# Optimization experiments

Measured on AMD Instinct MI355X. Metric: run time of the kernel, lower is better.

Reference implementation:

```python
import jax, jax.numpy as jnp
import numpy as np

# config
HIDDEN = 1024
NUM_EXPERTS = 16
TOP_K = 4
MOE_INTER = 512
NUM_SHARED = 2
SHARED_INTER = MOE_INTER * NUM_SHARED  # 1024
NORM_TOPK = True
ROUTED_SCALE = 1.0
NUM_TOKENS = 1024


def setup_inputs() -> dict:
    key = jax.random.key(0)
    ks = jax.random.split(key, 8)
    s = 0.02
    return {
        "hidden_states": jax.random.normal(ks[0], (NUM_TOKENS, HIDDEN), jnp.float32),
        # router (BailingMoEGate): weight [E, H], no bias
        "router_w": jax.random.normal(ks[1], (NUM_EXPERTS, HIDDEN), jnp.float32) * s,
        # routed experts: gate/up proj [E, H, I], down proj [E, I, H]
        "w_gate": jax.random.normal(ks[2], (NUM_EXPERTS, HIDDEN, MOE_INTER), jnp.float32) * s,
        "w_up": jax.random.normal(ks[3], (NUM_EXPERTS, HIDDEN, MOE_INTER), jnp.float32) * s,
        "w_down": jax.random.normal(ks[4], (NUM_EXPERTS, MOE_INTER, HIDDEN), jnp.float32) * s,
        # shared experts (BailingMoEMLP, merged gate_up): [H, 2*Is], [Is, H]
        "ws_gate_up": jax.random.normal(ks[5], (HIDDEN, 2 * SHARED_INTER), jnp.float32) * s,
        "ws_down": jax.random.normal(ks[6], (SHARED_INTER, HIDDEN), jnp.float32) * s,
    }


def _moe_forward(x, router_w, w_gate, w_up, w_down, ws_gate_up, ws_down):
    T = x.shape[0]
    # ---- router: logits -> softmax -> top-k (score_function='softmax', no bias)
    logits = jnp.einsum("th,eh->te", x, router_w)          # [T, E]
    probs = jax.nn.softmax(logits, axis=-1)
    topk_w, topk_idx = jax.lax.top_k(probs, TOP_K)         # [T, K]
    if NORM_TOPK:
        topk_w = topk_w / jnp.sum(topk_w, axis=-1, keepdims=True)
    topk_w = topk_w * ROUTED_SCALE
    # sparse combine weights [T, E] (zeros for non-selected experts)
    combine = jnp.zeros((T, NUM_EXPERTS), x.dtype).at[
        jnp.arange(T)[:, None], topk_idx
    ].set(topk_w.astype(x.dtype))
    # ---- routed experts: SiLU(x W_gate) * (x W_up) then W_down, weighted combine
    g = jnp.einsum("th,ehi->tei", x, w_gate)               # [T, E, I]
    u = jnp.einsum("th,ehi->tei", x, w_up)
    h = jax.nn.silu(g) * u
    routed = jnp.einsum("tei,eih,te->th", h, w_down, combine)
    # ---- shared experts (dense SwiGLU MLP)
    gu = x @ ws_gate_up                                    # [T, 2*Is]
    g_s, u_s = jnp.split(gu, 2, axis=-1)
    shared = (jax.nn.silu(g_s) * u_s) @ ws_down
    return routed + shared


def reference(hidden_states, router_w, w_gate, w_up, w_down, ws_gate_up, ws_down):
    return _moe_forward(hidden_states, router_w, w_gate, w_up, w_down,
                        ws_gate_up, ws_down)
```

## Files before the change

kernel.cpp:

```cpp
#include <hip/hip_runtime.h>
#include <stdint.h>


typedef __attribute__((ext_vector_type(8))) unsigned short ushort8;
typedef __attribute__((ext_vector_type(4))) float f32x4;
typedef __attribute__((ext_vector_type(8))) __bf16 bf16x8;

#define T_TOK 1024
#define HID   1024
#define NEXP  16
#define TOPK  4
#define MINTER 512
#define SINTER 1024

constexpr size_t WGU_E = 32 * 1024 * 32;
constexpr size_t WD_E  = 16 * 1024 * 32;

constexpr size_t OFF_COUNTS = 0;
constexpr size_t OFF_LIST   = 1024;
constexpr size_t OFF_WT     = OFF_LIST  + 65536;
constexpr size_t OFF_TIDX   = OFF_WT    + 65536;
constexpr size_t OFF_XB     = OFF_TIDX  + 65536;
constexpr size_t OFF_HR     = OFF_XB    + 2097152;
constexpr size_t OFF_HS     = OFF_HR    + 4194304;
constexpr size_t OFF_WGU    = OFF_HS    + 2097152;
constexpr size_t OFF_WD     = OFF_WGU   + 33554432;
constexpr size_t OFF_WSGU   = OFF_WD    + 16777216;
constexpr size_t OFF_WSD    = OFF_WSGU  + 4194304;
constexpr size_t OFF_ROUT   = OFF_WGU;

__device__ __forceinline__ unsigned short f2bf(float f) {
  union { float f; uint32_t u; } v; v.f = f;
  uint32_t r = (v.u + 0x7FFFu + ((v.u >> 16) & 1u)) >> 16;
  return (unsigned short)r;
}
__device__ __forceinline__ float bfu2f(uint32_t u) {
  union { uint32_t u; float f; } v; v.u = u << 16; return v.f;
}
__device__ __forceinline__ bf16x8 as_bf16x8(ushort8 s) {
  union { ushort8 s; bf16x8 b; } u; u.s = s; return u.b;
}
__device__ __forceinline__ float silu(float g) { return g / (1.f + __expf(-g)); }

__device__ __forceinline__ void glds16(const unsigned short* g, unsigned short* l) {
  __builtin_amdgcn_global_load_lds(
      (const __attribute__((address_space(1))) unsigned int*)g,
      (__attribute__((address_space(3))) unsigned int*)l, 16, 0, 0);
}

#define PIPE_BARRIER3() asm volatile("s_waitcnt vmcnt(3) lgkmcnt(0)\ns_barrier" ::: "memory")
#define PIPE_BARRIER0() asm volatile("s_waitcnt vmcnt(0) lgkmcnt(0)\ns_barrier" ::: "memory")

__global__ void init_kernel(int* counts) {
  if (threadIdx.x < NEXP) counts[threadIdx.x] = 0;
}

__global__ __launch_bounds__(64) void router_kernel(
    const float* __restrict__ x, const float* __restrict__ rw,
    int* counts, int* list, float* wt, int* tIdx,
    unsigned short* __restrict__ Xb) {
  const int t = blockIdx.x, l = threadIdx.x;
  float xv[16];
#pragma unroll
  for (int j = 0; j < 16; j++) xv[j] = x[t * HID + j * 64 + l];
#pragma unroll
  for (int j = 0; j < 16; j++) Xb[t * HID + j * 64 + l] = f2bf(xv[j]);
  float p[NEXP];
#pragma unroll
  for (int e = 0; e < NEXP; e++) {
    float s = 0.f;
#pragma unroll
    for (int j = 0; j < 16; j++) s += xv[j] * rw[e * HID + j * 64 + l];
#pragma unroll
    for (int off = 32; off > 0; off >>= 1) s += __shfl_xor(s, off);
    p[e] = s;
  }
  float mx = p[0];
#pragma unroll
  for (int e = 1; e < NEXP; e++) mx = fmaxf(mx, p[e]);
  int idx[TOPK]; float w4[TOPK]; float wsum = 0.f; unsigned used = 0u;
#pragma unroll
  for (int k = 0; k < TOPK; k++) {
    float bv = -1e30f; int bi = 0;
#pragma unroll
    for (int e = 0; e < NEXP; e++)
      if (!((used >> e) & 1u) && p[e] > bv) { bv = p[e]; bi = e; }
    used |= 1u << bi;
    idx[k] = bi;
    w4[k] = __expf(p[bi] - mx);
    wsum += w4[k];
  }
  const float inv = 1.f / wsum;
  if (l < TOPK) {
    const int e = idx[l];
    const int pos = atomicAdd(&counts[e], 1);
    list[e * 1024 + pos] = t;
    wt[e * 1024 + pos]   = w4[l] * inv;
    tIdx[t * TOPK + l]   = (e << 10) | pos;
  }
}

__global__ __launch_bounds__(256) void pack_all_kernel(
    const float* __restrict__ Wg, const float* __restrict__ Wu,
    const float* __restrict__ Wd, const float* __restrict__ Wsgu,
    const float* __restrict__ Wsd,
    unsigned short* __restrict__ WGUp, unsigned short* __restrict__ WDp,
    unsigned short* __restrict__ WSGUp, unsigned short* __restrict__ WSDp) {
  const int bid = blockIdx.x;
  const float* src; unsigned short* dst; int C, Nj, kp0, r0, c0, jbase, ilv;
  if (bid < 2048) {
    const int e = bid >> 7, loc = bid & 127, kt = loc >> 3, nt = loc & 7;
    src = Wg + (size_t)e * HID * MINTER; dst = WGUp + (size_t)e * WGU_E;
    C = MINTER; Nj = 1024; kp0 = 2 * kt; r0 = 64 * kt; c0 = 64 * nt;
    jbase = 128 * nt; ilv = 1;
  } else if (bid < 4096) {
    const int e = (bid - 2048) >> 7, loc = bid & 127, kt = loc >> 3, nt = loc & 7;
    src = Wu + (size_t)e * HID * MINTER; dst = WGUp + (size_t)e * WGU_E;
    C = MINTER; Nj = 1024; kp0 = 2 * kt; r0 = 64 * kt; c0 = 64 * nt;
    jbase = 128 * nt + 16; ilv = 1;
  } else if (bid < 6144) {
    const int e = (bid - 4096) >> 7, loc = bid & 127, kt = loc >> 4, nt = loc & 15;
    src = Wd + (size_t)e * MINTER * HID; dst = WDp + (size_t)e * WD_E;
    C = HID; Nj = 1024; kp0 = 2 * kt; r0 = 64 * kt; c0 = 64 * nt;
    jbase = 64 * nt; ilv = 0;
  } else if (bid < 6656) {
    const int loc = bid - 6144, kt = loc >> 5, nt = loc & 31;
    src = Wsgu; dst = WSGUp;
    C = 2048; Nj = 2048; kp0 = 2 * kt; r0 = 64 * kt; c0 = 64 * nt;
    const int isU = (nt >= 16), ntc = nt & 15;
    jbase = 128 * ntc + 16 * isU; ilv = 1;
  } else {
    const int loc = bid - 6656, kt = loc >> 4, nt = loc & 15;
    src = Wsd; dst = WSDp;
    C = HID; Nj = 1024; kp0 = 2 * kt; r0 = 64 * kt; c0 = 64 * nt;
    jbase = 64 * nt; ilv = 0;
  }
  __shared__ float tile[64][65];
  const int t = threadIdx.x;
  {
    const int r = t >> 4, c4 = (t & 15) * 4;
#pragma unroll
    for (int p = 0; p < 4; p++) {
      const int rr = p * 16 + r;
      const float4 v = *(const float4*)(src + (size_t)(r0 + rr) * C + c0 + c4);
      tile[rr][c4 + 0] = v.x; tile[rr][c4 + 1] = v.y;
      tile[rr][c4 + 2] = v.z; tile[rr][c4 + 3] = v.w;
    }
  }
  __syncthreads();
  {
    const int n = t >> 2, k8 = (t & 3) * 8;
    const int j = jbase + (ilv ? (32 * (n >> 4) + (n & 15)) : n);
#pragma unroll
    for (int h = 0; h < 2; h++) {
      const int k = 32 * h + k8;
      union { unsigned short u[8]; ushort8 v; } pk;
#pragma unroll
      for (int i = 0; i < 8; i++) pk.u[i] = f2bf(tile[k + i][n]);
      *(ushort8*)(dst + ((size_t)(kp0 + h) * Nj + j) * 32 + k8) = pk.v;
    }
  }
}

__global__ __launch_bounds__(256, 4) void phase1_kernel(
    const unsigned short* __restrict__ Xb,
    const unsigned short* __restrict__ WGUp,
    const unsigned short* __restrict__ WSGUp,
    const int* __restrict__ counts, const int* __restrict__ list,
    const float* __restrict__ wt,
    unsigned short* __restrict__ Hr,
    unsigned short* __restrict__ Hs) {
  const int z = blockIdx.z, x = blockIdx.x, y = blockIdx.y;
  const bool routed = (z < NEXP);
  int cnt = 0, base = 0;
  if (routed) {
    if (x >= 16) return;
    cnt = counts[z];
    if (y * 128 >= cnt) return;
#pragma unroll
    for (int i = 0; i < NEXP; i++) base += (i < z) ? counts[i] : 0;
  }
  __shared__ __align__(16) unsigned short sA[3][128 * 32];
  __shared__ __align__(16) unsigned short sB[3][64 * 32];
  const int tid = threadIdx.x, w = tid >> 6, l = tid & 63;
  const int wm = w >> 1, wn = w & 1, m0 = y * 128;
  const int swz = ((l & 3) ^ ((l >> 3) & 3)) * 8;
  const int Nj = routed ? 1024 : 2048;

  const unsigned short* aS[2];
#pragma unroll
  for (int ii = 0; ii < 2; ii++) {
    const int r = 32 * w + 16 * ii + (l >> 2);
    const unsigned short* row = routed
        ? Xb + (size_t)list[z * 1024 + min(m0 + r, cnt - 1)] * HID
        : Xb + (size_t)(m0 + r) * HID;
    aS[ii] = row + swz;
  }
  const unsigned short* pan = routed ? WGUp + (size_t)z * WGU_E : WSGUp;
  const unsigned short* bS = pan + ((size_t)(x * 64 + 16 * w + (l >> 2))) * 32 + swz;
  const size_t bStep = (size_t)Nj * 32;

  const int rsw = ((l >> 4) ^ (((l & 15) >> 1) & 3)) * 8;
  int aOff[4], bOff[2];
#pragma unroll
  for (int i = 0; i < 4; i++) aOff[i] = (wm * 64 + 16 * i + (l & 15)) * 32 + rsw;
#pragma unroll
  for (int jt = 0; jt < 2; jt++) bOff[jt] = (wn * 32 + 16 * jt + (l & 15)) * 32 + rsw;

  f32x4 acc[4][2];
#pragma unroll
  for (int i = 0; i < 4; i++)
#pragma unroll
    for (int jt = 0; jt < 2; jt++) acc[i][jt] = (f32x4){0.f, 0.f, 0.f, 0.f};

  auto stage = [&](int s, int b) {
    glds16(aS[0] + s * 32, &sA[b][(32 * w) * 32]);
    glds16(aS[1] + s * 32, &sA[b][(32 * w + 16) * 32]);
    glds16(bS + s * bStep, &sB[b][(16 * w) * 32]);
  };

  const int steps = HID / 32;
  stage(0, 0); stage(1, 1);
#pragma unroll 1
  for (int s = 0; s < steps; s++) {
    const int cb = s % 3;
    if (s + 2 < steps) { PIPE_BARRIER3(); stage(s + 2, (s + 2) % 3); }
    else if (s + 1 < steps) { PIPE_BARRIER3(); }
    else { PIPE_BARRIER0(); }
    const unsigned short* A = &sA[cb][0];
    const unsigned short* B = &sB[cb][0];
    bf16x8 af[4], bfr[2];
#pragma unroll
    for (int i = 0; i < 4; i++) af[i] = as_bf16x8(*(const ushort8*)(A + aOff[i]));
#pragma unroll
    for (int jt = 0; jt < 2; jt++) bfr[jt] = as_bf16x8(*(const ushort8*)(B + bOff[jt]));
#pragma unroll
    for (int jt = 0; jt < 2; jt++)
#pragma unroll
      for (int i = 0; i < 4; i++)
        acc[i][jt] = __builtin_amdgcn_mfma_f32_16x16x32_bf16(af[i], bfr[jt], acc[i][jt], 0, 0, 0);
  }

  const int rl = (l >> 4) * 4, pc = 16 * wn + (l & 15);
#pragma unroll
  for (int i = 0; i < 4; i++)
#pragma unroll
    for (int r = 0; r < 4; r++) {
      const int grow = m0 + wm * 64 + 16 * i + rl + r;
      const float g = acc[i][0][r], u = acc[i][1][r];
      if (routed) {
        if (grow < cnt) {
          const float h = silu(g) * u * wt[z * 1024 + grow];
          Hr[((size_t)x * 4096 + base + grow) * 32 + pc] = f2bf(h);
        }
      } else {
        const float h = silu(g) * u;
        Hs[((size_t)x * 1024 + grow) * 32 + pc] = f2bf(h);
      }
    }
}

__global__ __launch_bounds__(256, 4) void phase2_kernel(
    const unsigned short* __restrict__ Hr, const unsigned short* __restrict__ Hs,
    const unsigned short* __restrict__ WDp, const unsigned short* __restrict__ WSDp,
    const int* __restrict__ counts,
    unsigned short* __restrict__ Rout,
    float* __restrict__ out) {
  const int z = blockIdx.z, x = blockIdx.x, y = blockIdx.y;
  const bool routed = (z < NEXP);
  int cnt = 0, base = 0, steps;
  if (routed) {
    cnt = counts[z];
    if (y * 128 >= cnt) return;
#pragma unroll
    for (int i = 0; i < NEXP; i++) base += (i < z) ? counts[i] : 0;
    steps = MINTER / 32;
  } else {
    steps = SINTER / 32;
  }
  __shared__ __align__(16) unsigned short sA[3][128 * 32];
  __shared__ __align__(16) unsigned short sB[3][64 * 32];
  const int tid = threadIdx.x, w = tid >> 6, l = tid & 63;
  const int wm = w >> 1, wn = w & 1, m0 = y * 128;
  const int swz = ((l & 3) ^ ((l >> 3) & 3)) * 8;
  const size_t aStep = (size_t)(routed ? 4096 : 1024) * 32;

  const unsigned short* aS[2];
#pragma unroll
  for (int ii = 0; ii < 2; ii++) {
    const int r = 32 * w + 16 * ii + (l >> 2);
    const int R = routed ? (base + min(m0 + r, cnt - 1)) : (m0 + r);
    aS[ii] = (routed ? Hr : Hs) + (size_t)R * 32 + swz;
  }
  const unsigned short* pan = routed ? WDp + (size_t)z * WD_E : WSDp;
  const unsigned short* bS = pan + ((size_t)(x * 64 + 16 * w + (l >> 2))) * 32 + swz;
  const size_t bStep = (size_t)1024 * 32;

  const int rsw = ((l >> 4) ^ (((l & 15) >> 1) & 3)) * 8;
  int aOff[4], bOff[2];
#pragma unroll
  for (int i = 0; i < 4; i++) aOff[i] = (wm * 64 + 16 * i + (l & 15)) * 32 + rsw;
#pragma unroll
  for (int jt = 0; jt < 2; jt++) bOff[jt] = (wn * 32 + 16 * jt + (l & 15)) * 32 + rsw;

  f32x4 acc[4][2];
#pragma unroll
  for (int i = 0; i < 4; i++)
#pragma unroll
    for (int jt = 0; jt < 2; jt++) acc[i][jt] = (f32x4){0.f, 0.f, 0.f, 0.f};

  auto stage = [&](int s, int b) {
    glds16(aS[0] + s * aStep, &sA[b][(32 * w) * 32]);
    glds16(aS[1] + s * aStep, &sA[b][(32 * w + 16) * 32]);
    glds16(bS + s * bStep, &sB[b][(16 * w) * 32]);
  };

  stage(0, 0); stage(1, 1);
#pragma unroll 1
  for (int s = 0; s < steps; s++) {
    const int cb = s % 3;
    if (s + 2 < steps) { PIPE_BARRIER3(); stage(s + 2, (s + 2) % 3); }
    else if (s + 1 < steps) { PIPE_BARRIER3(); }
    else { PIPE_BARRIER0(); }
    const unsigned short* A = &sA[cb][0];
    const unsigned short* B = &sB[cb][0];
    bf16x8 af[4], bfr[2];
#pragma unroll
    for (int i = 0; i < 4; i++) af[i] = as_bf16x8(*(const ushort8*)(A + aOff[i]));
#pragma unroll
    for (int jt = 0; jt < 2; jt++) bfr[jt] = as_bf16x8(*(const ushort8*)(B + bOff[jt]));
#pragma unroll
    for (int jt = 0; jt < 2; jt++)
#pragma unroll
      for (int i = 0; i < 4; i++)
        acc[i][jt] = __builtin_amdgcn_mfma_f32_16x16x32_bf16(af[i], bfr[jt], acc[i][jt], 0, 0, 0);
  }

  const int rl = (l >> 4) * 4;
#pragma unroll
  for (int i = 0; i < 4; i++)
#pragma unroll
    for (int r = 0; r < 4; r++) {
      const int grow = m0 + wm * 64 + 16 * i + rl + r;
#pragma unroll
      for (int jt = 0; jt < 2; jt++) {
        const int col = 64 * x + 32 * wn + 16 * jt + (l & 15);
        if (routed) {
          if (grow < cnt)
            Rout[(size_t)(base + grow) * HID + col] = f2bf(acc[i][jt][r]);
        } else {
          out[(size_t)grow * HID + col] = acc[i][jt][r];
        }
      }
    }
}

__global__ __launch_bounds__(256) void combine_kernel(
    const unsigned short* __restrict__ Rout, const int* __restrict__ counts,
    const int* __restrict__ tIdx, float* __restrict__ out) {
  __shared__ int sb[NEXP];
  if (threadIdx.x == 0) {
    int s = 0;
#pragma unroll
    for (int e = 0; e < NEXP; e++) { sb[e] = s; s += counts[e]; }
  }
  __syncthreads();
  const int t = blockIdx.x, c4 = threadIdx.x * 4;
  float4 o = *(const float4*)(out + (size_t)t * HID + c4);
#pragma unroll
  for (int k = 0; k < TOPK; k++) {
    const int v = tIdx[t * TOPK + k];
    const int row = sb[v >> 10] + (v & 1023);
    const uint2 rv = *(const uint2*)(Rout + (size_t)row * HID + c4);
    o.x += bfu2f(rv.x & 0xffffu); o.y += bfu2f(rv.x >> 16);
    o.z += bfu2f(rv.y & 0xffffu); o.w += bfu2f(rv.y >> 16);
  }
  *(float4*)(out + (size_t)t * HID + c4) = o;
}

extern "C" void kernel_launch(void* const* d_in, const int* in_sizes, int n_in,
                              void* d_out, int out_size, void* d_ws, size_t ws_size,
                              hipStream_t stream) {
  const float* x      = (const float*)d_in[0];
  const float* rw     = (const float*)d_in[1];
  const float* w_gate = (const float*)d_in[2];
  const float* w_up   = (const float*)d_in[3];
  const float* w_down = (const float*)d_in[4];
  const float* ws_gu  = (const float*)d_in[5];
  const float* ws_dn  = (const float*)d_in[6];
  float* out = (float*)d_out;
  char* ws = (char*)d_ws;

  int*   counts = (int*)  (ws + OFF_COUNTS);
  int*   list   = (int*)  (ws + OFF_LIST);
  float* wtbuf  = (float*)(ws + OFF_WT);
  int*   tIdx   = (int*)  (ws + OFF_TIDX);
  unsigned short* Xb    = (unsigned short*)(ws + OFF_XB);
  unsigned short* Hr    = (unsigned short*)(ws + OFF_HR);
  unsigned short* Hs    = (unsigned short*)(ws + OFF_HS);
  unsigned short* WGUp  = (unsigned short*)(ws + OFF_WGU);
  unsigned short* WDp   = (unsigned short*)(ws + OFF_WD);
  unsigned short* WSGUp = (unsigned short*)(ws + OFF_WSGU);
  unsigned short* WSDp  = (unsigned short*)(ws + OFF_WSD);
  unsigned short* Rout  = (unsigned short*)(ws + OFF_ROUT);

  init_kernel<<<1, 64, 0, stream>>>(counts);
  router_kernel<<<T_TOK, 64, 0, stream>>>(x, rw, counts, list, wtbuf, tIdx, Xb);
  pack_all_kernel<<<6912, 256, 0, stream>>>(
      w_gate, w_up, w_down, ws_gu, ws_dn, WGUp, WDp, WSGUp, WSDp);
  phase1_kernel<<<dim3(32, 8, 17), 256, 0, stream>>>(
      Xb, WGUp, WSGUp, counts, list, wtbuf, Hr, Hs);
  phase2_kernel<<<dim3(16, 8, 17), 256, 0, stream>>>(
      Hr, Hs, WDp, WSDp, counts, Rout, out);
  combine_kernel<<<T_TOK, 256, 0, stream>>>(Rout, counts, tIdx, out);
  (void)in_sizes; (void)n_in; (void)out_size; (void)ws_size;
}
```

Before: 243.4 us.

## Shrink GEMM tiles to 64x64 with 2-wave blocks and 4-stage pipeline

Both expert GEMM kernels drop from 128x64 tiles with 4 waves to 64x64 tiles with 2 waves per block, doubling the y grid. The global-to-LDS pipeline deepens from 3 to 4 buffers with matching vmcnt waits. The aim is finer granularity for experts with few tokens, less padding waste and more blocks to fill the CUs. In exchange, each block reuses the weight tiles across fewer rows, so weight traffic from memory and L2 rises.

Measured after the change: 261.4 us. 1.07x slower.

```diff
diff --git a/kernel.cpp b/kernel.cpp
--- a/kernel.cpp
+++ b/kernel.cpp
@@ -48,7 +48,8 @@
       (__attribute__((address_space(3))) unsigned int*)l, 16, 0, 0);
 }
 
-#define PIPE_BARRIER3() asm volatile("s_waitcnt vmcnt(3) lgkmcnt(0)\ns_barrier" ::: "memory")
+#define PIPE_BARRIER8() asm volatile("s_waitcnt vmcnt(8) lgkmcnt(0)\ns_barrier" ::: "memory")
+#define PIPE_BARRIER4() asm volatile("s_waitcnt vmcnt(4) lgkmcnt(0)\ns_barrier" ::: "memory")
 #define PIPE_BARRIER0() asm volatile("s_waitcnt vmcnt(0) lgkmcnt(0)\ns_barrier" ::: "memory")
 
 __global__ void init_kernel(int* counts) {
@@ -162,7 +163,7 @@
   }
 }
 
-__global__ __launch_bounds__(256, 4) void phase1_kernel(
+__global__ __launch_bounds__(128, 3) void phase1_kernel(
     const unsigned short* __restrict__ Xb,
     const unsigned short* __restrict__ WGUp,
     const unsigned short* __restrict__ WSGUp,
@@ -176,14 +177,14 @@
   if (routed) {
     if (x >= 16) return;
     cnt = counts[z];
-    if (y * 128 >= cnt) return;
+    if (y * 64 >= cnt) return;
 #pragma unroll
     for (int i = 0; i < NEXP; i++) base += (i < z) ? counts[i] : 0;
   }
-  __shared__ __align__(16) unsigned short sA[3][128 * 32];
-  __shared__ __align__(16) unsigned short sB[3][64 * 32];
+  __shared__ __align__(16) unsigned short sA[4][64 * 32];
+  __shared__ __align__(16) unsigned short sB[4][64 * 32];
   const int tid = threadIdx.x, w = tid >> 6, l = tid & 63;
-  const int wm = w >> 1, wn = w & 1, m0 = y * 128;
+  const int wn = w, m0 = y * 64;
   const int swz = ((l & 3) ^ ((l >> 3) & 3)) * 8;
   const int Nj = routed ? 1024 : 2048;
 
@@ -197,15 +198,18 @@
     aS[ii] = row + swz;
   }
   const unsigned short* pan = routed ? WGUp + (size_t)z * WGU_E : WSGUp;
-  const unsigned short* bS = pan + ((size_t)(x * 64 + 16 * w + (l >> 2))) * 32 + swz;
+  const unsigned short* bS[2];
+#pragma unroll
+  for (int ii = 0; ii < 2; ii++)
+    bS[ii] = pan + ((size_t)(x * 64 + 32 * w + 16 * ii + (l >> 2))) * 32 + swz;
   const size_t bStep = (size_t)Nj * 32;
 
   const int rsw = ((l >> 4) ^ (((l & 15) >> 1) & 3)) * 8;
   int aOff[4], bOff[2];
 #pragma unroll
-  for (int i = 0; i < 4; i++) aOff[i] = (wm * 64 + 16 * i + (l & 15)) * 32 + rsw;
-#pragma unroll
-  for (int jt = 0; jt < 2; jt++) bOff[jt] = (wn * 32 + 16 * jt + (l & 15)) * 32 + rsw;
+  for (int i = 0; i < 4; i++) aOff[i] = (16 * i + (l & 15)) * 32 + rsw;
+#pragma unroll
+  for (int jt = 0; jt < 2; jt++) bOff[jt] = (32 * wn + 16 * jt + (l & 15)) * 32 + rsw;
 
   f32x4 acc[4][2];
 #pragma unroll
@@ -216,17 +220,19 @@
   auto stage = [&](int s, int b) {
     glds16(aS[0] + s * 32, &sA[b][(32 * w) * 32]);
     glds16(aS[1] + s * 32, &sA[b][(32 * w + 16) * 32]);
-    glds16(bS + s * bStep, &sB[b][(16 * w) * 32]);
+    glds16(bS[0] + s * bStep, &sB[b][(32 * w) * 32]);
+    glds16(bS[1] + s * bStep, &sB[b][(32 * w + 16) * 32]);
   };
 
   const int steps = HID / 32;
-  stage(0, 0); stage(1, 1);
+  stage(0, 0); stage(1, 1); stage(2, 2);
 #pragma unroll 1
   for (int s = 0; s < steps; s++) {
-    const int cb = s % 3;
-    if (s + 2 < steps) { PIPE_BARRIER3(); stage(s + 2, (s + 2) % 3); }
-    else if (s + 1 < steps) { PIPE_BARRIER3(); }
-    else { PIPE_BARRIER0(); }
+    const int cb = s & 3;
+    if (s + 3 < steps)       { PIPE_BARRIER8(); stage(s + 3, (s + 3) & 3); }
+    else if (s + 3 == steps) { PIPE_BARRIER8(); }
+    else if (s + 2 == steps) { PIPE_BARRIER4(); }
+    else                     { PIPE_BARRIER0(); }
     const unsigned short* A = &sA[cb][0];
     const unsigned short* B = &sB[cb][0];
     bf16x8 af[4], bfr[2];
@@ -246,7 +252,7 @@
   for (int i = 0; i < 4; i++)
 #pragma unroll
     for (int r = 0; r < 4; r++) {
-      const int grow = m0 + wm * 64 + 16 * i + rl + r;
+      const int grow = m0 + 16 * i + rl + r;
       const float g = acc[i][0][r], u = acc[i][1][r];
       if (routed) {
         if (grow < cnt) {
@@ -260,7 +266,7 @@
     }
 }
 
-__global__ __launch_bounds__(256, 4) void phase2_kernel(
+__global__ __launch_bounds__(128, 3) void phase2_kernel(
     const unsigned short* __restrict__ Hr, const unsigned short* __restrict__ Hs,
     const unsigned short* __restrict__ WDp, const unsigned short* __restrict__ WSDp,
     const int* __restrict__ counts,
@@ -271,17 +277,17 @@
   int cnt = 0, base = 0, steps;
   if (routed) {
     cnt = counts[z];
-    if (y * 128 >= cnt) return;
+    if (y * 64 >= cnt) return;
 #pragma unroll
     for (int i = 0; i < NEXP; i++) base += (i < z) ? counts[i] : 0;
     steps = MINTER / 32;
   } else {
     steps = SINTER / 32;
   }
-  __shared__ __align__(16) unsigned short sA[3][128 * 32];
-  __shared__ __align__(16) unsigned short sB[3][64 * 32];
+  __shared__ __align__(16) unsigned short sA[4][64 * 32];
+  __shared__ __align__(16) unsigned short sB[4][64 * 32];
   const int tid = threadIdx.x, w = tid >> 6, l = tid & 63;
-  const int wm = w >> 1, wn = w & 1, m0 = y * 128;
+  const int wn = w, m0 = y * 64;
   const int swz = ((l & 3) ^ ((l >> 3) & 3)) * 8;
   const size_t aStep = (size_t)(routed ? 4096 : 1024) * 32;
 
@@ -293,15 +299,18 @@
     aS[ii] = (routed ? Hr : Hs) + (size_t)R * 32 + swz;
   }
   const unsigned short* pan = routed ? WDp + (size_t)z * WD_E : WSDp;
-  const unsigned short* bS = pan + ((size_t)(x * 64 + 16 * w + (l >> 2))) * 32 + swz;
+  const unsigned short* bS[2];
+#pragma unroll
+  for (int ii = 0; ii < 2; ii++)
+    bS[ii] = pan + ((size_t)(x * 64 + 32 * w + 16 * ii + (l >> 2))) * 32 + swz;
   const size_t bStep = (size_t)1024 * 32;
 
   const int rsw = ((l >> 4) ^ (((l & 15) >> 1) & 3)) * 8;
   int aOff[4], bOff[2];
 #pragma unroll
-  for (int i = 0; i < 4; i++) aOff[i] = (wm * 64 + 16 * i + (l & 15)) * 32 + rsw;
-#pragma unroll
-  for (int jt = 0; jt < 2; jt++) bOff[jt] = (wn * 32 + 16 * jt + (l & 15)) * 32 + rsw;
+  for (int i = 0; i < 4; i++) aOff[i] = (16 * i + (l & 15)) * 32 + rsw;
+#pragma unroll
+  for (int jt = 0; jt < 2; jt++) bOff[jt] = (32 * wn + 16 * jt + (l & 15)) * 32 + rsw;
 
   f32x4 acc[4][2];
 #pragma unroll
@@ -312,16 +321,18 @@
   auto stage = [&](int s, int b) {
     glds16(aS[0] + s * aStep, &sA[b][(32 * w) * 32]);
     glds16(aS[1] + s * aStep, &sA[b][(32 * w + 16) * 32]);
-    glds16(bS + s * bStep, &sB[b][(16 * w) * 32]);
+    glds16(bS[0] + s * bStep, &sB[b][(32 * w) * 32]);
+    glds16(bS[1] + s * bStep, &sB[b][(32 * w + 16) * 32]);
   };
 
-  stage(0, 0); stage(1, 1);
+  stage(0, 0); stage(1, 1); stage(2, 2);
 #pragma unroll 1
   for (int s = 0; s < steps; s++) {
-    const int cb = s % 3;
-    if (s + 2 < steps) { PIPE_BARRIER3(); stage(s + 2, (s + 2) % 3); }
-    else if (s + 1 < steps) { PIPE_BARRIER3(); }
-    else { PIPE_BARRIER0(); }
+    const int cb = s & 3;
+    if (s + 3 < steps)       { PIPE_BARRIER8(); stage(s + 3, (s + 3) & 3); }
+    else if (s + 3 == steps) { PIPE_BARRIER8(); }
+    else if (s + 2 == steps) { PIPE_BARRIER4(); }
+    else                     { PIPE_BARRIER0(); }
     const unsigned short* A = &sA[cb][0];
     const unsigned short* B = &sB[cb][0];
     bf16x8 af[4], bfr[2];
@@ -341,7 +352,7 @@
   for (int i = 0; i < 4; i++)
 #pragma unroll
     for (int r = 0; r < 4; r++) {
-      const int grow = m0 + wm * 64 + 16 * i + rl + r;
+      const int grow = m0 + 16 * i + rl + r;
 #pragma unroll
       for (int jt = 0; jt < 2; jt++) {
         const int col = 64 * x + 32 * wn + 16 * jt + (l & 15);
@@ -408,9 +419,9 @@
   router_kernel<<<T_TOK, 64, 0, stream>>>(x, rw, counts, list, wtbuf, tIdx, Xb);
   pack_all_kernel<<<6912, 256, 0, stream>>>(
       w_gate, w_up, w_down, ws_gu, ws_dn, WGUp, WDp, WSGUp, WSDp);
-  phase1_kernel<<<dim3(32, 8, 17), 256, 0, stream>>>(
+  phase1_kernel<<<dim3(32, 16, 17), 128, 0, stream>>>(
       Xb, WGUp, WSGUp, counts, list, wtbuf, Hr, Hs);
-  phase2_kernel<<<dim3(16, 8, 17), 256, 0, stream>>>(
+  phase2_kernel<<<dim3(16, 16, 17), 128, 0, stream>>>(
       Hr, Hs, WDp, WSDp, counts, Rout, out);
   combine_kernel<<<T_TOK, 256, 0, stream>>>(Rout, counts, tIdx, out);
   (void)in_sizes; (void)n_in; (void)out_size; (void)ws_size;
```
